# Kernel tuning notes

Measured on AMD Instinct MI355X. Metric: run time of the kernel, lower is better.

The kernel has to match this reference:

```python
import jax, jax.numpy as jnp
import numpy as np

N_TEMPS = 800
TEMP_STEP = 0.00125
TARGET_VAL = 0.2666666667
TOL = 0.01


def setup_inputs() -> dict:
    key = jax.random.key(0)
    logits = jax.random.normal(key, (128, 1000), dtype=jnp.float32)
    return {"logits": logits}


def reference(logits) -> jnp.ndarray:
    B, C = logits.shape
    dt = logits.dtype
    # ECE-style 3-bin boundaries: linspace(0, 1, 4)
    bin_lowers = jnp.array([0.0, 1.0 / 3.0, 2.0 / 3.0], dtype=dt)
    bin_uppers = jnp.array([1.0 / 3.0, 2.0 / 3.0, 1.0], dtype=dt)
    new_bin_lowers = jnp.array([0.8, 0.86666666666, 0.93333333333], dtype=dt)

    # original confidence = max softmax prob per sample
    conf = jnp.max(jax.nn.softmax(logits, axis=1), axis=1)  # [B]

    # bin assignment: uppers > conf and lowers <= conf
    in_bin = (bin_uppers[None, :] > conf[:, None]) & (bin_lowers[None, :] <= conf[:, None])
    bin_idx = jnp.argmax(in_bin, axis=1)  # [B]

    # target confidence after compression
    new_conf = new_bin_lowers[bin_idx] + (1.0 / 15.0) * ((conf - bin_lowers[bin_idx]) / TARGET_VAL)  # [B]

    # temperature grid 1.0, 0.99875, ... (800 values)
    temps = 1.0 - TEMP_STEP * jnp.arange(N_TEMPS, dtype=dt)  # [T]

    # vectorized sweep: scaled logits [B, T, C]
    scaled = logits[:, None, :] / temps[None, :, None]
    # max softmax prob = exp(max_logit - logsumexp)
    conf_t = jnp.exp(jnp.max(scaled, axis=-1) - jax.nn.logsumexp(scaled, axis=-1))  # [B, T]

    ok = jnp.abs(conf_t - new_conf[:, None]) <= TOL  # [B, T]
    found = jnp.any(ok, axis=1)                      # [B]
    j_first = jnp.argmax(ok, axis=1)                 # first matching temperature index
    chosen_temp = temps[j_first]                     # [B]

    out = jnp.where(found[:, None], logits / chosen_temp[:, None], logits)
    return out
```

## Files before the change

### kernel.cpp

```cpp
#include <hip/hip_runtime.h>
#include <math.h>

#define NB 128
#define NC 1000
#define NT 800

__device__ __forceinline__ float block_reduce_sum(float v, float* sred, float* sbcast) {
    for (int o = 32; o > 0; o >>= 1) v += __shfl_xor(v, o, 64);
    int tid = threadIdx.x;
    if ((tid & 63) == 0) sred[tid >> 6] = v;
    __syncthreads();
    if (tid == 0) *sbcast = (sred[0] + sred[1]) + (sred[2] + sred[3]);
    __syncthreads();
    return *sbcast;
}

__device__ __forceinline__ float eval_S(const float* __restrict__ srow, float t, float m,
                                        float* sred, float* sbcast) {
    float m2 = m / t;
    float s = 0.f;
    for (int i = threadIdx.x; i < NC; i += 256)
        s += expf(srow[i] / t - m2);
    return block_reduce_sum(s, sred, sbcast);
}

__device__ __forceinline__ float conft_from_S(float S, float t, float m) {
    float m2 = t == 1.0f ? m : (m / t);
    float lse = m2 + logf(S);
    return expf(m2 - lse);
}

__global__ __launch_bounds__(256) void logitcomp_kernel(const float* __restrict__ logits,
                                                        float* __restrict__ out) {
    __shared__ float srow[NC];
    __shared__ float sred[4];
    __shared__ float sbcast;

    int r = blockIdx.x;
    int tid = threadIdx.x;
    const float* row = logits + r * NC;

    for (int i = tid; i < NC; i += 256) srow[i] = row[i];
    __syncthreads();

    float mv = -INFINITY;
    for (int i = tid; i < NC; i += 256) mv = fmaxf(mv, srow[i]);
    for (int o = 32; o > 0; o >>= 1) mv = fmaxf(mv, __shfl_xor(mv, o, 64));
    if ((tid & 63) == 0) sred[tid >> 6] = mv;
    __syncthreads();
    if (tid == 0) sbcast = fmaxf(fmaxf(sred[0], sred[1]), fmaxf(sred[2], sred[3]));
    __syncthreads();
    float m = sbcast;

    float S1 = eval_S(srow, 1.0f, m, sred, &sbcast);
    float conf = 1.0f / S1;

    const float third = (float)(1.0 / 3.0);
    const float twoth = (float)(2.0 / 3.0);
    bool b0 = (third > conf) && (0.0f <= conf);
    bool b1 = (twoth > conf) && (third <= conf);
    bool b2 = (1.0f > conf) && (twoth <= conf);
    int idx = b0 ? 0 : (b1 ? 1 : (b2 ? 2 : 0));
    float bl = (idx == 0) ? 0.0f : ((idx == 1) ? third : twoth);
    float nb = (idx == 0) ? 0.8f : ((idx == 1) ? (float)0.86666666666 : (float)0.93333333333);
    const float TARGET = (float)0.2666666667;
    const float K = (float)(1.0 / 15.0);
    float nc = nb + K * ((conf - bl) / TARGET);

    int lo = 0, count = NT;
    while (count > 0) {
        int step = count >> 1;
        int mid = lo + step;
        float t = 1.0f - 0.00125f * (float)mid;
        float S = eval_S(srow, t, m, sred, &sbcast);
        float conft = conft_from_S(S, t, m);
        bool ok = fabsf(conft - nc) <= 0.01f;
        bool below = (conft < nc) && !ok;
        if (below) { lo = mid + 1; count -= step + 1; }
        else        count = step;
    }

    bool found = false;
    float tch = 1.0f;
    if (lo < NT) {
        float t = 1.0f - 0.00125f * (float)lo;
        float S = eval_S(srow, t, m, sred, &sbcast);
        float conft = conft_from_S(S, t, m);
        found = fabsf(conft - nc) <= 0.01f;
        tch = t;
    }

    float* orow = out + r * NC;
    for (int i = tid; i < NC; i += 256) {
        float l = srow[i];
        orow[i] = found ? (l / tch) : l;
    }
}

extern "C" void kernel_launch(void* const* d_in, const int* in_sizes, int n_in,
                              void* d_out, int out_size, void* d_ws, size_t ws_size,
                              hipStream_t stream) {
    const float* logits = (const float*)d_in[0];
    float* out = (float*)d_out;
    logitcomp_kernel<<<NB, 256, 0, stream>>>(logits, out);
}
```

Measured before the change: 64.56 us.

## Replace per-row binary search with parallel full temperature sweep across three kernels

The sequential binary search over 800 temperatures (about 10 dependent block-wide reductions per row on 128 blocks) is replaced by a brute-force sweep. Each wave evaluates 8 temperatures at once using exp2 with fused multiply-add, and an atomicMin keeps the first matching index. A prep kernel computes the row max and target confidence, and a write kernel applies the chosen temperature. This exposes far more parallelism across 3200 blocks at the cost of much more total exp work and two extra kernel launches. It also matches the reference's first-match semantics exactly instead of relying on monotonicity.

```diff
diff --git a/kernel.cpp b/kernel.cpp
--- a/kernel.cpp
+++ b/kernel.cpp
@@ -3,97 +3,126 @@
 
 #define NB 128
 #define NC 1000
+#define NC4 250
 #define NT 800
+#define LOG2E 1.4426950408889634f
 
-__device__ __forceinline__ float block_reduce_sum(float v, float* sred, float* sbcast) {
-    for (int o = 32; o > 0; o >>= 1) v += __shfl_xor(v, o, 64);
-    int tid = threadIdx.x;
-    if ((tid & 63) == 0) sred[tid >> 6] = v;
-    __syncthreads();
-    if (tid == 0) *sbcast = (sred[0] + sred[1]) + (sred[2] + sred[3]);
-    __syncthreads();
-    return *sbcast;
-}
 
-__device__ __forceinline__ float eval_S(const float* __restrict__ srow, float t, float m,
-                                        float* sred, float* sbcast) {
-    float m2 = m / t;
-    float s = 0.f;
-    for (int i = threadIdx.x; i < NC; i += 256)
-        s += expf(srow[i] / t - m2);
-    return block_reduce_sum(s, sred, sbcast);
-}
-
-__device__ __forceinline__ float conft_from_S(float S, float t, float m) {
-    float m2 = t == 1.0f ? m : (m / t);
-    float lse = m2 + logf(S);
-    return expf(m2 - lse);
-}
-
-__global__ __launch_bounds__(256) void logitcomp_kernel(const float* __restrict__ logits,
-                                                        float* __restrict__ out) {
-    __shared__ float srow[NC];
+__global__ __launch_bounds__(256) void prep_kernel(const float* __restrict__ logits,
+                                                   float* __restrict__ wm,
+                                                   float* __restrict__ wnc,
+                                                   int* __restrict__ wminj) {
     __shared__ float sred[4];
-    __shared__ float sbcast;
-
+    __shared__ float sb;
     int r = blockIdx.x;
     int tid = threadIdx.x;
-    const float* row = logits + r * NC;
+    const float4* row4 = (const float4*)(logits + r * NC);
 
-    for (int i = tid; i < NC; i += 256) srow[i] = row[i];
-    __syncthreads();
-
+    float4 v = make_float4(0.f, 0.f, 0.f, 0.f);
+    bool act = tid < NC4;
     float mv = -INFINITY;
-    for (int i = tid; i < NC; i += 256) mv = fmaxf(mv, srow[i]);
+    if (act) {
+        v = row4[tid];
+        mv = fmaxf(fmaxf(v.x, v.y), fmaxf(v.z, v.w));
+    }
     for (int o = 32; o > 0; o >>= 1) mv = fmaxf(mv, __shfl_xor(mv, o, 64));
     if ((tid & 63) == 0) sred[tid >> 6] = mv;
     __syncthreads();
-    if (tid == 0) sbcast = fmaxf(fmaxf(sred[0], sred[1]), fmaxf(sred[2], sred[3]));
+    if (tid == 0) sb = fmaxf(fmaxf(sred[0], sred[1]), fmaxf(sred[2], sred[3]));
     __syncthreads();
-    float m = sbcast;
+    float m = sb;
 
-    float S1 = eval_S(srow, 1.0f, m, sred, &sbcast);
-    float conf = 1.0f / S1;
+    float s = 0.f;
+    if (act) s = expf(v.x - m) + expf(v.y - m) + expf(v.z - m) + expf(v.w - m);
+    for (int o = 32; o > 0; o >>= 1) s += __shfl_xor(s, o, 64);
+    if ((tid & 63) == 0) sred[tid >> 6] = s;
+    __syncthreads();
+    if (tid == 0) {
+        float S1 = (sred[0] + sred[1]) + (sred[2] + sred[3]);
+        float conf = 1.0f / S1;
 
-    const float third = (float)(1.0 / 3.0);
-    const float twoth = (float)(2.0 / 3.0);
-    bool b0 = (third > conf) && (0.0f <= conf);
-    bool b1 = (twoth > conf) && (third <= conf);
-    bool b2 = (1.0f > conf) && (twoth <= conf);
-    int idx = b0 ? 0 : (b1 ? 1 : (b2 ? 2 : 0));
-    float bl = (idx == 0) ? 0.0f : ((idx == 1) ? third : twoth);
-    float nb = (idx == 0) ? 0.8f : ((idx == 1) ? (float)0.86666666666 : (float)0.93333333333);
-    const float TARGET = (float)0.2666666667;
-    const float K = (float)(1.0 / 15.0);
-    float nc = nb + K * ((conf - bl) / TARGET);
+        const float third = (float)(1.0 / 3.0);
+        const float twoth = (float)(2.0 / 3.0);
+        bool b0 = (third > conf) && (0.0f <= conf);
+        bool b1 = (twoth > conf) && (third <= conf);
+        bool b2 = (1.0f > conf) && (twoth <= conf);
+        int idx = b0 ? 0 : (b1 ? 1 : (b2 ? 2 : 0));
+        float bl = (idx == 0) ? 0.0f : ((idx == 1) ? third : twoth);
+        float nb = (idx == 0) ? 0.8f : ((idx == 1) ? (float)0.86666666666 : (float)0.93333333333);
+        float nc = nb + (float)(1.0 / 15.0) * ((conf - bl) / (float)0.2666666667);
 
-    int lo = 0, count = NT;
-    while (count > 0) {
-        int step = count >> 1;
-        int mid = lo + step;
-        float t = 1.0f - 0.00125f * (float)mid;
-        float S = eval_S(srow, t, m, sred, &sbcast);
-        float conft = conft_from_S(S, t, m);
-        bool ok = fabsf(conft - nc) <= 0.01f;
-        bool below = (conft < nc) && !ok;
-        if (below) { lo = mid + 1; count -= step + 1; }
-        else        count = step;
+        wm[r] = m;
+        wnc[r] = nc;
+        wminj[r] = NT;
+    }
+}
+
+__global__ __launch_bounds__(256) void sweep_kernel(const float* __restrict__ logits,
+                                                    const float* __restrict__ wm,
+                                                    const float* __restrict__ wnc,
+                                                    int* __restrict__ wminj) {
+    int r = blockIdx.y;
+    int tid = threadIdx.x;
+    int wave = tid >> 6;
+    int lane = tid & 63;
+    int j0 = blockIdx.x * 32 + wave * 8;
+
+    float m = wm[r];
+    float nc = wnc[r];
+
+    float a[8], b[8], s[8];
+#pragma unroll
+    for (int k = 0; k < 8; ++k) {
+        float t = 1.0f - 0.00125f * (float)(j0 + k);
+        a[k] = LOG2E / t;
+        b[k] = -(m * a[k]);
+        s[k] = 0.f;
     }
 
-    bool found = false;
-    float tch = 1.0f;
-    if (lo < NT) {
-        float t = 1.0f - 0.00125f * (float)lo;
-        float S = eval_S(srow, t, m, sred, &sbcast);
-        float conft = conft_from_S(S, t, m);
-        found = fabsf(conft - nc) <= 0.01f;
-        tch = t;
+    const float4* row4 = (const float4*)(logits + r * NC);
+    for (int i = lane; i < NC4; i += 64) {
+        float4 v = row4[i];
+#pragma unroll
+        for (int k = 0; k < 8; ++k) {
+            s[k] += exp2f(fmaf(v.x, a[k], b[k]));
+            s[k] += exp2f(fmaf(v.y, a[k], b[k]));
+            s[k] += exp2f(fmaf(v.z, a[k], b[k]));
+            s[k] += exp2f(fmaf(v.w, a[k], b[k]));
+        }
     }
 
-    float* orow = out + r * NC;
-    for (int i = tid; i < NC; i += 256) {
-        float l = srow[i];
-        orow[i] = found ? (l / tch) : l;
+#pragma unroll
+    for (int k = 0; k < 8; ++k)
+        for (int o = 32; o > 0; o >>= 1) s[k] += __shfl_xor(s[k], o, 64);
+
+    if (lane == 0) {
+#pragma unroll
+        for (int k = 0; k < 8; ++k) {
+            float conft = expf(-logf(s[k]));
+            if (fabsf(conft - nc) <= 0.01f) atomicMin(&wminj[r], j0 + k);
+        }
+    }
+}
+
+__global__ __launch_bounds__(256) void write_kernel(const float* __restrict__ logits,
+                                                    const int* __restrict__ wminj,
+                                                    float* __restrict__ out) {
+    int r = blockIdx.x;
+    int tid = threadIdx.x;
+    int mj = wminj[r];
+    bool found = mj < NT;
+    float tch = found ? (1.0f - 0.00125f * (float)mj) : 1.0f;
+
+    const float4* row4 = (const float4*)(logits + r * NC);
+    float4* orow4 = (float4*)(out + r * NC);
+    if (tid < NC4) {
+        float4 v = row4[tid];
+        float4 o;
+        o.x = found ? v.x / tch : v.x;
+        o.y = found ? v.y / tch : v.y;
+        o.z = found ? v.z / tch : v.z;
+        o.w = found ? v.w / tch : v.w;
+        orow4[tid] = o;
     }
 }
 
@@ -102,5 +131,12 @@
                               hipStream_t stream) {
     const float* logits = (const float*)d_in[0];
     float* out = (float*)d_out;
-    logitcomp_kernel<<<NB, 256, 0, stream>>>(logits, out);
+
+    float* wm = (float*)d_ws;
+    float* wnc = wm + NB;
+    int* wminj = (int*)(wnc + NB);
+
+    prep_kernel<<<NB, 256, 0, stream>>>(logits, wm, wnc, wminj);
+    sweep_kernel<<<dim3(NT / 32, NB), 256, 0, stream>>>(logits, wm, wnc, wminj);
+    write_kernel<<<NB, 256, 0, stream>>>(logits, wminj, out);
 }
```

Result: slower. 86.70 us (+34.3%).

## Replace serial binary search with two-level 64-way parallel temperature probing

Applied to the files above, without the earlier changes.

The sequential binary search over 800 temperatures (about ten dependent block-wide reductions) becomes two rounds of 64 parallel probes. A coarse stride-13 sweep is followed by a fine sweep of 64 consecutive temperatures, each lane of a 1024-thread block evaluating one temperature, with ballot picking the first non-below index. The exp is rewritten as exp2 of an fma with a precomputed scale, and loads and stores are vectorized to float4. This cuts the serial chain of reductions and barriers, but keeps the same monotonicity assumption as the binary search and does more total exp work per row.

```diff
diff --git a/kernel.cpp b/kernel.cpp
--- a/kernel.cpp
+++ b/kernel.cpp
@@ -3,56 +3,61 @@
 
 #define NB 128
 #define NC 1000
+#define NC4 250
 #define NT 800
+#define NW 16
+#define THREADS 1024
+#define LOG2E 1.4426950408889634f
 
-__device__ __forceinline__ float block_reduce_sum(float v, float* sred, float* sbcast) {
-    for (int o = 32; o > 0; o >>= 1) v += __shfl_xor(v, o, 64);
-    int tid = threadIdx.x;
-    if ((tid & 63) == 0) sred[tid >> 6] = v;
-    __syncthreads();
-    if (tid == 0) *sbcast = (sred[0] + sred[1]) + (sred[2] + sred[3]);
-    __syncthreads();
-    return *sbcast;
+__device__ __forceinline__ float probe_sum(const float4* __restrict__ srow4, int w,
+                                           float a, float b) {
+    float s = 0.f;
+#pragma unroll 4
+    for (int i = w; i < NC4; i += NW) {
+        float4 v = srow4[i];
+        s += exp2f(fmaf(v.x, a, b));
+        s += exp2f(fmaf(v.y, a, b));
+        s += exp2f(fmaf(v.z, a, b));
+        s += exp2f(fmaf(v.w, a, b));
+    }
+    return s;
 }
 
-__device__ __forceinline__ float eval_S(const float* __restrict__ srow, float t, float m,
-                                        float* sred, float* sbcast) {
-    float m2 = m / t;
-    float s = 0.f;
-    for (int i = threadIdx.x; i < NC; i += 256)
-        s += expf(srow[i] / t - m2);
-    return block_reduce_sum(s, sred, sbcast);
-}
+__global__ __launch_bounds__(THREADS) void logitcomp_kernel(const float* __restrict__ logits,
+                                                            float* __restrict__ out) {
+    __shared__ float4 srow4[NC4];
+    __shared__ float part[NW][64];
+    __shared__ float wred[NW];
+    __shared__ float wred2[NW];
 
-__device__ __forceinline__ float conft_from_S(float S, float t, float m) {
-    float m2 = t == 1.0f ? m : (m / t);
-    float lse = m2 + logf(S);
-    return expf(m2 - lse);
-}
+    const int tid = threadIdx.x;
+    const int w = tid >> 6;
+    const int lane = tid & 63;
+    const int r = blockIdx.x;
+    const float4* row4 = (const float4*)(logits + r * NC);
 
-__global__ __launch_bounds__(256) void logitcomp_kernel(const float* __restrict__ logits,
-                                                        float* __restrict__ out) {
-    __shared__ float srow[NC];
-    __shared__ float sred[4];
-    __shared__ float sbcast;
+    float4 v0 = make_float4(0.f, 0.f, 0.f, 0.f);
+    float mv = -INFINITY;
+    if (tid < NC4) {
+        v0 = row4[tid];
+        srow4[tid] = v0;
+        mv = fmaxf(fmaxf(v0.x, v0.y), fmaxf(v0.z, v0.w));
+    }
+    for (int o = 32; o > 0; o >>= 1) mv = fmaxf(mv, __shfl_xor(mv, o, 64));
+    if (lane == 0) wred[w] = mv;
+    __syncthreads();
+    float m = wred[0];
+#pragma unroll
+    for (int k = 1; k < NW; ++k) m = fmaxf(m, wred[k]);
 
-    int r = blockIdx.x;
-    int tid = threadIdx.x;
-    const float* row = logits + r * NC;
-
-    for (int i = tid; i < NC; i += 256) srow[i] = row[i];
+    float s1 = 0.f;
+    if (tid < NC4) s1 = expf(v0.x - m) + expf(v0.y - m) + expf(v0.z - m) + expf(v0.w - m);
+    for (int o = 32; o > 0; o >>= 1) s1 += __shfl_xor(s1, o, 64);
+    if (lane == 0) wred2[w] = s1;
     __syncthreads();
-
-    float mv = -INFINITY;
-    for (int i = tid; i < NC; i += 256) mv = fmaxf(mv, srow[i]);
-    for (int o = 32; o > 0; o >>= 1) mv = fmaxf(mv, __shfl_xor(mv, o, 64));
-    if ((tid & 63) == 0) sred[tid >> 6] = mv;
-    __syncthreads();
-    if (tid == 0) sbcast = fmaxf(fmaxf(sred[0], sred[1]), fmaxf(sred[2], sred[3]));
-    __syncthreads();
-    float m = sbcast;
-
-    float S1 = eval_S(srow, 1.0f, m, sred, &sbcast);
+    float S1 = 0.f;
+#pragma unroll
+    for (int k = 0; k < NW; ++k) S1 += wred2[k];
     float conf = 1.0f / S1;
 
     const float third = (float)(1.0 / 3.0);
@@ -63,37 +68,64 @@
     int idx = b0 ? 0 : (b1 ? 1 : (b2 ? 2 : 0));
     float bl = (idx == 0) ? 0.0f : ((idx == 1) ? third : twoth);
     float nb = (idx == 0) ? 0.8f : ((idx == 1) ? (float)0.86666666666 : (float)0.93333333333);
-    const float TARGET = (float)0.2666666667;
-    const float K = (float)(1.0 / 15.0);
-    float nc = nb + K * ((conf - bl) / TARGET);
+    float nc = nb + (float)(1.0 / 15.0) * ((conf - bl) / (float)0.2666666667);
 
-    int lo = 0, count = NT;
-    while (count > 0) {
-        int step = count >> 1;
-        int mid = lo + step;
-        float t = 1.0f - 0.00125f * (float)mid;
-        float S = eval_S(srow, t, m, sred, &sbcast);
-        float conft = conft_from_S(S, t, m);
-        bool ok = fabsf(conft - nc) <= 0.01f;
-        bool below = (conft < nc) && !ok;
-        if (below) { lo = mid + 1; count -= step + 1; }
-        else        count = step;
+    int j1 = min(13 * lane, NT - 1);
+    float t1 = 1.0f - 0.00125f * (float)j1;
+    float a1 = LOG2E / t1;
+    float b1c = -(m * a1);
+    float sA = probe_sum(srow4, w, a1, b1c);
+    part[w][lane] = sA;
+    __syncthreads();
+    float SA = 0.f;
+#pragma unroll
+    for (int k = 0; k < NW; ++k) SA += part[k][lane];
+    float cA = expf(-logf(SA));
+    bool okA = fabsf(cA - nc) <= 0.01f;
+    bool belowA = (cA < nc) && !okA;
+    unsigned long long nbm = __ballot(!belowA);
+
+    int lo = 0;
+    if (nbm != 0ull) {
+        int pstar = (int)__ffsll(nbm) - 1;
+        lo = (pstar == 0) ? 0 : (13 * (pstar - 1) + 1);
     }
+
+    __syncthreads();
+    int j2 = min(lo + lane, NT - 1);
+    float t2 = 1.0f - 0.00125f * (float)j2;
+    float a2 = LOG2E / t2;
+    float b2c = -(m * a2);
+    float sB = probe_sum(srow4, w, a2, b2c);
+    part[w][lane] = sB;
+    __syncthreads();
+    float SB = 0.f;
+#pragma unroll
+    for (int k = 0; k < NW; ++k) SB += part[k][lane];
+    float cB = expf(-logf(SB));
+    bool okB = fabsf(cB - nc) <= 0.01f;
+    bool belowB = (cB < nc) && !okB;
+    unsigned long long nbm2 = __ballot(!belowB);
+    unsigned long long okm2 = __ballot(okB);
 
     bool found = false;
     float tch = 1.0f;
-    if (lo < NT) {
-        float t = 1.0f - 0.00125f * (float)lo;
-        float S = eval_S(srow, t, m, sred, &sbcast);
-        float conft = conft_from_S(S, t, m);
-        found = fabsf(conft - nc) <= 0.01f;
-        tch = t;
+    if (nbm != 0ull && nbm2 != 0ull) {
+        int q = (int)__ffsll(nbm2) - 1;
+        int jstar = min(lo + q, NT - 1);
+        found = ((okm2 >> q) & 1ull) != 0ull;
+        tch = 1.0f - 0.00125f * (float)jstar;
     }
 
-    float* orow = out + r * NC;
-    for (int i = tid; i < NC; i += 256) {
-        float l = srow[i];
-        orow[i] = found ? (l / tch) : l;
+    float4* orow4 = (float4*)(out + r * NC);
+    if (tid < NC4) {
+        float4 v = srow4[tid];
+        float4 o;
+        o.x = found ? v.x / tch : v.x;
+        o.y = found ? v.y / tch : v.y;
+        o.z = found ? v.z / tch : v.z;
+        o.w = found ? v.w / tch : v.w;
+        orow4[tid] = o;
     }
 }
 
@@ -102,5 +134,5 @@
                               hipStream_t stream) {
     const float* logits = (const float*)d_in[0];
     float* out = (float*)d_out;
-    logitcomp_kernel<<<NB, 256, 0, stream>>>(logits, out);
+    logitcomp_kernel<<<NB, THREADS, 0, stream>>>(logits, out);
 }
```

Measured after the change: 61.83 us. -4.2%, faster.
